# Optimization experiments

Measured on AMD Instinct MI355X. Metric: run time of the kernel, lower is better.

The kernel has to match this reference:

```python
import jax, jax.numpy as jnp
import numpy as np

HEADS, DK, S, SIGMA = 8, 64, 48, 5.0  # d_model=512, query/key spatial 48x48


def setup_inputs() -> dict:
    rng = jax.random.key(0)
    ks = jax.random.split(rng, 8)
    b, n, d = 2, S * S, HEADS * DK
    sc = 0.03  # keep pre-softmax scores in a sane range
    return {
        "query": jax.random.normal(ks[0], (b, n, d), jnp.float32),
        "key": jax.random.normal(ks[1], (b, n, d), jnp.float32),
        "value0": jax.random.uniform(ks[2], (b, n), jnp.float32),
        "value1": jax.random.uniform(ks[3], (b, n), jnp.float32),
        "Wq": jax.random.normal(ks[4], (d, d), jnp.float32) * sc,
        "bq": jax.random.normal(ks[5], (d,), jnp.float32) * sc,
        "Wk": jax.random.normal(ks[6], (d, d), jnp.float32) * sc,
        "bk": jax.random.normal(ks[7], (d,), jnp.float32) * sc,
    }


def _apply_gaussian_kernel(corr):
    # corr: [B, hw, S, S]  (B = b*heads, hw = S*S query positions)
    B = corr.shape[0]
    idx = jnp.argmax(corr, axis=1)                       # [B, S, S] best query index per key pos
    idx_y = (idx // S).astype(corr.dtype)[:, None, None, :, :]  # [B,1,1,S,S]
    idx_x = (idx % S).astype(corr.dtype)[:, None, None, :, :]
    lin = jnp.linspace(-1.0, 1.0, S).astype(corr.dtype)
    x = lin.reshape(1, 1, S, 1, 1)
    y = lin.reshape(1, S, 1, 1, 1)
    # faithful to source: linspace grid vs integer argmax coords
    gk = jnp.exp(-((x - idx_x) ** 2 + (y - idx_y) ** 2) / (2.0 * SIGMA ** 2))  # [B,S,S,S,S]
    return gk.reshape(B, S * S, S, S) * corr


def reference(query, key, value0, value1, Wq, bq, Wk, bk):
    b, nq, d = query.shape
    q = (query @ Wq.T + bq).reshape(b, nq, HEADS, DK).transpose(0, 2, 1, 3)  # [b,h,nq,dk]
    k = (key @ Wk.T + bk).reshape(b, -1, HEADS, DK).transpose(0, 2, 1, 3)    # [b,h,nk,dk]
    scores = jnp.einsum('bhqd,bhkd->bhqk', q, k)                             # [b,h,nq,nk]
    B = b * HEADS
    corr = _apply_gaussian_kernel(scores.reshape(B, nq, S, S))
    scores = corr.reshape(b, HEADS, nq, nq) / jnp.sqrt(jnp.asarray(DK, scores.dtype))
    attn = jax.nn.softmax(scores, axis=-1)
    x0 = jnp.einsum('bhqk,bk->bhq', attn, value0)   # attn @ value0
    x1 = jnp.einsum('bhqk,bq->bhk', attn, value1)   # attn^T @ value1
    # outer product per head, then mean over heads -> [b,nq,nk]
    return jnp.einsum('bhq,bhk->bqk', x0, x1) / HEADS
```

## Files before the change

kernel.cpp:

```cpp
#include <hip/hip_runtime.h>
#include <cstddef>
#include <cstdint>

namespace {

constexpr int S = 48;
constexpr int N = S * S;
constexpr int D = 512;
constexpr int DK = 64;
constexpr int B = 2;
constexpr int BH = 16;
constexpr int BHN = BH * N;
constexpr int G_ARG = 9;
constexpr int CH_ARG = N / G_ARG;
constexpr int G_RC = 6;
constexpr int CH_RC = N / G_RC;
constexpr float SCALE = 0.125f;
constexpr float INV2S2 = 0.02f;

typedef __attribute__((ext_vector_type(8))) short short8;
typedef __attribute__((ext_vector_type(8))) unsigned short ushort8v;
typedef __attribute__((ext_vector_type(4))) float f32x4;

#define MFMA(a, b, c) __builtin_amdgcn_mfma_f32_16x16x32_bf16((a), (b), (c), 0, 0, 0)

struct U3 { ushort a, b, c; };

__device__ __forceinline__ U3 split3(float x)
{
    U3 u;
    uint b1 = __float_as_uint(x);
    uint r1 = (b1 + (0x7FFFu + ((b1 >> 16) & 1u))) & 0xFFFF0000u;
    u.a = (ushort)(r1 >> 16);
    float d1 = x - __uint_as_float(r1);
    uint b2 = __float_as_uint(d1);
    uint r2 = (b2 + (0x7FFFu + ((b2 >> 16) & 1u))) & 0xFFFF0000u;
    u.b = (ushort)(r2 >> 16);
    float d2 = d1 - __uint_as_float(r2);
    uint b3 = __float_as_uint(d2);
    u.c = (ushort)((b3 + (0x7FFFu + ((b3 >> 16) & 1u))) >> 16);
    return u;
}

__device__ __forceinline__ void stage_async(ushort* __restrict__ L,
                                            const ushort* __restrict__ g, int tid)
{
    #pragma unroll
    for (int it = 0; it < 2; it++) {
        int f = tid + 256 * it;
        int row = f >> 3, c8 = (f & 7) * 8;
        int srcoff = row * 64 + (c8 ^ ((row & 7) << 3));
        ushort* lbase = L + (size_t)(f & ~63) * 8;
        __builtin_amdgcn_global_load_lds(
            (const __attribute__((address_space(1))) void*)(g + srcoff),
            (__attribute__((address_space(3))) void*)lbase, 16, 0, 0);
    }
}

__device__ __forceinline__ short8 frag_swz(const ushort* __restrict__ L, int row, int k)
{
    int off = row * 64 + (k ^ ((row & 7) << 3));
    return *(const short8*)&L[off];
}

__device__ __forceinline__ short8 gfrag(const ushort* __restrict__ p, size_t off)
{
    return *(const short8*)&p[off];
}

__global__ __launch_bounds__(256)
void split_kernel(const float* __restrict__ qin, const float* __restrict__ kin,
                  const float* __restrict__ Wq, const float* __restrict__ Wk,
                  ushort* __restrict__ XQ1, ushort* __restrict__ XQ2, ushort* __restrict__ XQ3,
                  ushort* __restrict__ XK1, ushort* __restrict__ XK2, ushort* __restrict__ XK3,
                  ushort* __restrict__ W1, ushort* __restrict__ W2, ushort* __restrict__ W3)
{
    const int z = blockIdx.y;
    const int gid = blockIdx.x * 256 + threadIdx.x;
    const float* src;
    ushort *O1, *O2, *O3;
    size_t dst, soff;
    if (z < 2) {
        int m = gid >> 6, c = gid & 63;
        int b = (m >= N) ? 1 : 0;
        int npos = m - b * N;
        src = z ? kin : qin;
        if (z) { O1 = XK1; O2 = XK2; O3 = XK3; }
        else   { O1 = XQ1; O2 = XQ2; O3 = XQ3; }
        soff = (size_t)m * D + c * 8;
        dst = ((size_t)(b * 8 + (c >> 3)) * N + npos) * 64 + (c & 7) * 8;
    } else {
        if (gid >= 65536) return;
        int r = gid >> 6, c = gid & 63;
        int inp = r >> 9, n = r & 511;
        src = inp ? Wk : Wq;
        O1 = W1; O2 = W2; O3 = W3;
        soff = (size_t)n * D + c * 8;
        dst = ((size_t)(inp * 8 + (c >> 3)) * 512 + n) * 64 + (c & 7) * 8;
    }
    ushort8v u1, u2, u3;
    #pragma unroll
    for (int j = 0; j < 8; j++) {
        U3 t = split3(src[soff + j]);
        u1[j] = t.a; u2[j] = t.b; u3[j] = t.c;
    }
    *(ushort8v*)&O1[dst] = u1;
    *(ushort8v*)&O2[dst] = u2;
    *(ushort8v*)&O3[dst] = u3;
}

__global__ __launch_bounds__(256)
void proj_kernel(const ushort* __restrict__ X1, const ushort* __restrict__ X2,
                 const ushort* __restrict__ X3, const ushort* __restrict__ Wp1,
                 const ushort* __restrict__ Wp2, const ushort* __restrict__ Wp3,
                 const float* __restrict__ bias,
                 ushort* __restrict__ O1, ushort* __restrict__ O2, ushort* __restrict__ O3)
{
    const int tid = threadIdx.x;
    const int lane = tid & 63, w = tid >> 6;
    const int wm = w >> 1, wn = w & 1;
    const int lg = lane >> 4, ln = lane & 15;
    const int hsel = blockIdx.x;
    const int my = blockIdx.y;
    const int b = my / 36;
    const int npos0 = (my % 36) * 64;

    __shared__ alignas(16) ushort bufX[3][64 * 64];
    __shared__ alignas(16) ushort bufW[3][64 * 64];

    f32x4 acc[2][2];
    #pragma unroll
    for (int mt = 0; mt < 2; mt++)
        #pragma unroll
        for (int nt = 0; nt < 2; nt++) acc[mt][nt] = (f32x4){0.f, 0.f, 0.f, 0.f};

    for (int kh = 0; kh < 8; kh++) {
        stage_async(bufX[0], X1 + ((size_t)(b * 8 + kh) * N + npos0) * 64, tid);
        stage_async(bufX[1], X2 + ((size_t)(b * 8 + kh) * N + npos0) * 64, tid);
        stage_async(bufX[2], X3 + ((size_t)(b * 8 + kh) * N + npos0) * 64, tid);
        stage_async(bufW[0], Wp1 + ((size_t)kh * 512 + hsel * 64) * 64, tid);
        stage_async(bufW[1], Wp2 + ((size_t)kh * 512 + hsel * 64) * 64, tid);
        stage_async(bufW[2], Wp3 + ((size_t)kh * 512 + hsel * 64) * 64, tid);
        __syncthreads();

        short8 A[3][2][2], Bv[3][2][2];
        #pragma unroll
        for (int mt = 0; mt < 2; mt++)
            #pragma unroll
            for (int c = 0; c < 2; c++) {
                int row = 32 * wm + 16 * mt + ln, k = 32 * c + 8 * lg;
                A[0][mt][c] = frag_swz(bufX[0], row, k);
                A[1][mt][c] = frag_swz(bufX[1], row, k);
                A[2][mt][c] = frag_swz(bufX[2], row, k);
            }
        #pragma unroll
        for (int nt = 0; nt < 2; nt++)
            #pragma unroll
            for (int c = 0; c < 2; c++) {
                int row = 32 * wn + 16 * nt + ln, k = 32 * c + 8 * lg;
                Bv[0][nt][c] = frag_swz(bufW[0], row, k);
                Bv[1][nt][c] = frag_swz(bufW[1], row, k);
                Bv[2][nt][c] = frag_swz(bufW[2], row, k);
            }
        #pragma unroll
        for (int mt = 0; mt < 2; mt++)
            #pragma unroll
            for (int nt = 0; nt < 2; nt++) {
                f32x4 a = acc[mt][nt];
                a = MFMA(A[0][mt][0], Bv[0][nt][0], a);
                a = MFMA(A[0][mt][1], Bv[0][nt][1], a);
                a = MFMA(A[0][mt][0], Bv[1][nt][0], a);
                a = MFMA(A[0][mt][1], Bv[1][nt][1], a);
                a = MFMA(A[1][mt][0], Bv[0][nt][0], a);
                a = MFMA(A[1][mt][1], Bv[0][nt][1], a);
                a = MFMA(A[0][mt][0], Bv[2][nt][0], a);
                a = MFMA(A[0][mt][1], Bv[2][nt][1], a);
                a = MFMA(A[1][mt][0], Bv[1][nt][0], a);
                a = MFMA(A[1][mt][1], Bv[1][nt][1], a);
                a = MFMA(A[2][mt][0], Bv[0][nt][0], a);
                a = MFMA(A[2][mt][1], Bv[0][nt][1], a);
                acc[mt][nt] = a;
            }
        __syncthreads();
    }
    float* Cs = (float*)&bufX[0][0];
    #pragma unroll
    for (int mt = 0; mt < 2; mt++)
        #pragma unroll
        for (int nt = 0; nt < 2; nt++)
            #pragma unroll
            for (int r = 0; r < 4; r++)
                Cs[(32 * wm + 16 * mt + 4 * lg + r) * 68 + 32 * wn + 16 * nt + ln] =
                    acc[mt][nt][r];
    __syncthreads();
    const int row = tid >> 2, c0 = (tid & 3) * 16;
    size_t dst = ((size_t)(b * 8 + hsel) * N + npos0 + row) * 64 + c0;
    #pragma unroll
    for (int half = 0; half < 2; half++) {
        ushort8v u1, u2, u3;
        #pragma unroll
        for (int j = 0; j < 8; j++) {
            int cc = c0 + half * 8 + j;
            float v = Cs[row * 68 + cc] + bias[hsel * 64 + cc];
            U3 t = split3(v);
            u1[j] = t.a; u2[j] = t.b; u3[j] = t.c;
        }
        *(ushort8v*)&O1[dst + half * 8] = u1;
        *(ushort8v*)&O2[dst + half * 8] = u2;
        *(ushort8v*)&O3[dst + half * 8] = u3;
    }
}

__global__ __launch_bounds__(256)
void argmax_kernel(const ushort* __restrict__ Q1, const ushort* __restrict__ Q2,
                   const ushort* __restrict__ Q3, const ushort* __restrict__ K1,
                   const ushort* __restrict__ K2, const ushort* __restrict__ K3,
                   float* __restrict__ argV, int* __restrict__ argQ)
{
    const int bh = blockIdx.y;
    const int g  = blockIdx.z;
    const int tid = threadIdx.x;
    const int w = tid >> 6, lane = tid & 63;
    const int lg = lane >> 4, ln = lane & 15;
    const int kb = blockIdx.x * 128 + w * 32;
    const size_t hb = (size_t)bh * N;

    __shared__ alignas(16) ushort buf[3][64 * 64];

    short8 A[3][2][2];
    #pragma unroll
    for (int mt = 0; mt < 2; mt++)
        #pragma unroll
        for (int c = 0; c < 2; c++) {
            size_t off = (hb + kb + 16 * mt + ln) * 64 + 32 * c + 8 * lg;
            A[0][mt][c] = gfrag(K1, off);
            A[1][mt][c] = gfrag(K2, off);
            A[2][mt][c] = gfrag(K3, off);
        }

    float bestv[2][4];
    int   bestq[2][4];
    #pragma unroll
    for (int mt = 0; mt < 2; mt++)
        #pragma unroll
        for (int r = 0; r < 4; r++) { bestv[mt][r] = -3e38f; bestq[mt][r] = 0; }

    for (int qt = g * CH_ARG; qt < (g + 1) * CH_ARG; qt += 64) {
        stage_async(buf[0], Q1 + (hb + qt) * 64, tid);
        stage_async(buf[1], Q2 + (hb + qt) * 64, tid);
        stage_async(buf[2], Q3 + (hb + qt) * 64, tid);
        __syncthreads();
        #pragma unroll
        for (int nt = 0; nt < 4; nt++) {
            short8 Bv0[2], Bv1[2], Bv2[2];
            #pragma unroll
            for (int c = 0; c < 2; c++) {
                int row = 16 * nt + ln, k = 32 * c + 8 * lg;
                Bv0[c] = frag_swz(buf[0], row, k);
                Bv1[c] = frag_swz(buf[1], row, k);
                Bv2[c] = frag_swz(buf[2], row, k);
            }
            const int q = qt + 16 * nt + ln;
            #pragma unroll
            for (int mt = 0; mt < 2; mt++) {
                f32x4 acc = {0.f, 0.f, 0.f, 0.f};
                acc = MFMA(A[0][mt][0], Bv0[0], acc);
                acc = MFMA(A[0][mt][1], Bv0[1], acc);
                acc = MFMA(A[0][mt][0], Bv1[0], acc);
                acc = MFMA(A[0][mt][1], Bv1[1], acc);
                acc = MFMA(A[1][mt][0], Bv0[0], acc);
                acc = MFMA(A[1][mt][1], Bv0[1], acc);
                acc = MFMA(A[0][mt][0], Bv2[0], acc);
                acc = MFMA(A[0][mt][1], Bv2[1], acc);
                acc = MFMA(A[1][mt][0], Bv1[0], acc);
                acc = MFMA(A[1][mt][1], Bv1[1], acc);
                acc = MFMA(A[2][mt][0], Bv0[0], acc);
                acc = MFMA(A[2][mt][1], Bv0[1], acc);
                #pragma unroll
                for (int r = 0; r < 4; r++)
                    if (acc[r] > bestv[mt][r]) { bestv[mt][r] = acc[r]; bestq[mt][r] = q; }
            }
        }
        __syncthreads();
    }
    #pragma unroll
    for (int d = 1; d < 16; d <<= 1) {
        #pragma unroll
        for (int mt = 0; mt < 2; mt++)
            #pragma unroll
            for (int r = 0; r < 4; r++) {
                float ov = __shfl_xor(bestv[mt][r], d);
                int   oq = __shfl_xor(bestq[mt][r], d);
                if (ov > bestv[mt][r] || (ov == bestv[mt][r] && oq < bestq[mt][r])) {
                    bestv[mt][r] = ov; bestq[mt][r] = oq;
                }
            }
    }
    if (ln == 0) {
        #pragma unroll
        for (int mt = 0; mt < 2; mt++)
            #pragma unroll
            for (int r = 0; r < 4; r++) {
                size_t o = (size_t)g * BHN + hb + kb + 16 * mt + 4 * lg + r;
                argV[o] = bestv[mt][r];
                argQ[o] = bestq[mt][r];
            }
    }
}

__global__ __launch_bounds__(256)
void argcombine_kernel(const float* __restrict__ argV, const int* __restrict__ argQ,
                       int* __restrict__ idxout)
{
    int i = blockIdx.x * 256 + threadIdx.x;
    if (i >= BHN) return;
    float bv = argV[i]; int bq = argQ[i];
    #pragma unroll
    for (int g = 1; g < G_ARG; g++) {
        float v = argV[(size_t)g * BHN + i];
        int   q = argQ[(size_t)g * BHN + i];
        if (v > bv) { bv = v; bq = q; }
    }
    idxout[i] = bq;
}

__global__ __launch_bounds__(256)
void rowpass_kernel(const ushort* __restrict__ Q1, const ushort* __restrict__ Q2,
                    const ushort* __restrict__ K1, const ushort* __restrict__ K2,
                    const int* __restrict__ idxbuf, const float* __restrict__ value0,
                    float* __restrict__ rowPl, float* __restrict__ rowPa)
{
    const int bh = blockIdx.y, b = bh >> 3;
    const int g = blockIdx.z;
    const int tid = threadIdx.x;
    const int w = tid >> 6, lane = tid & 63;
    const int lg = lane >> 4, ln = lane & 15;
    const int qb = blockIdx.x * 128 + w * 32;
    const size_t hb = (size_t)bh * N;

    __shared__ alignas(16) ushort buf[2][64 * 64];
    __shared__ float F[48][49];
    __shared__ int ixi[64], iyi[64];
    __shared__ float v0s[64];

    for (int i = tid; i < 48 * 48; i += 256) {
        int a = i / 48, j = i % 48;
        float lj = -1.0f + (2.0f / 47.0f) * (float)j;
        float dd = lj - (float)a;
        F[a][j] = __expf(-dd * dd * INV2S2);
    }

    short8 Bq[2][2][2];
    int qx_[2], qy_[2];
    #pragma unroll
    for (int nt = 0; nt < 2; nt++) {
        #pragma unroll
        for (int c = 0; c < 2; c++) {
            size_t off = (hb + qb + 16 * nt + ln) * 64 + 32 * c + 8 * lg;
            Bq[0][nt][c] = gfrag(Q1, off);
            Bq[1][nt][c] = gfrag(Q2, off);
        }
        int qq = qb + 16 * nt + ln;
        qx_[nt] = qq % 48; qy_[nt] = qq / 48;
    }
    __syncthreads();

    float l[2] = {0.f, 0.f}, a0[2] = {0.f, 0.f};

    for (int kt = g * CH_RC; kt < (g + 1) * CH_RC; kt += 64) {
        stage_async(buf[0], K1 + (hb + kt) * 64, tid);
        stage_async(buf[1], K2 + (hb + kt) * 64, tid);
        if (tid < 64) {
            int v = idxbuf[hb + kt + tid];
            ixi[tid] = v % 48; iyi[tid] = v / 48;
            v0s[tid] = value0[(size_t)b * N + kt + tid];
        }
        __syncthreads();
        #pragma unroll
        for (int mt = 0; mt < 4; mt++) {
            short8 A0[2], A1[2];
            #pragma unroll
            for (int c = 0; c < 2; c++) {
                int row = 16 * mt + ln, k = 32 * c + 8 * lg;
                A0[c] = frag_swz(buf[0], row, k);
                A1[c] = frag_swz(buf[1], row, k);
            }
            #pragma unroll
            for (int nt = 0; nt < 2; nt++) {
                f32x4 acc = {0.f, 0.f, 0.f, 0.f};
                acc = MFMA(A0[0], Bq[0][nt][0], acc);
                acc = MFMA(A0[1], Bq[0][nt][1], acc);
                acc = MFMA(A0[0], Bq[1][nt][0], acc);
                acc = MFMA(A0[1], Bq[1][nt][1], acc);
                acc = MFMA(A1[0], Bq[0][nt][0], acc);
                acc = MFMA(A1[1], Bq[0][nt][1], acc);
                #pragma unroll
                for (int r = 0; r < 4; r++) {
                    int kl = 16 * mt + 4 * lg + r;
                    float s = acc[r] * F[ixi[kl]][qx_[nt]] * F[iyi[kl]][qy_[nt]] * SCALE;
                    float e = __expf(s);
                    l[nt]  += e;
                    a0[nt] += e * v0s[kl];
                }
            }
        }
        __syncthreads();
    }
    #pragma unroll
    for (int d = 16; d < 64; d <<= 1) {
        #pragma unroll
        for (int nt = 0; nt < 2; nt++) {
            l[nt]  += __shfl_xor(l[nt], d);
            a0[nt] += __shfl_xor(a0[nt], d);
        }
    }
    if (lane < 16) {
        #pragma unroll
        for (int nt = 0; nt < 2; nt++) {
            size_t o = (size_t)g * BHN + hb + qb + 16 * nt + ln;
            rowPl[o] = l[nt];
            rowPa[o] = a0[nt];
        }
    }
}

__global__ __launch_bounds__(256)
void rowfinal_kernel(const float* __restrict__ rowPl, const float* __restrict__ rowPa,
                     float* __restrict__ denomo, float* __restrict__ x0o)
{
    int i = blockIdx.x * 256 + threadIdx.x;
    if (i >= BHN) return;
    float L = 0.f, A = 0.f;
    #pragma unroll
    for (int g = 0; g < G_RC; g++) {
        L += rowPl[(size_t)g * BHN + i];
        A += rowPa[(size_t)g * BHN + i];
    }
    denomo[i] = L;
    x0o[i] = A / L;
}

__global__ __launch_bounds__(256)
void colpass_kernel(const ushort* __restrict__ Q1, const ushort* __restrict__ Q2,
                    const ushort* __restrict__ K1, const ushort* __restrict__ K2,
                    const int* __restrict__ idxbuf, const float* __restrict__ value1,
                    const float* __restrict__ denomo, float* __restrict__ colP)
{
    const int bh = blockIdx.y, b = bh >> 3;
    const int g = blockIdx.z;
    const int tid = threadIdx.x;
    const int w = tid >> 6, lane = tid & 63;
    const int lg = lane >> 4, ln = lane & 15;
    const int kb = blockIdx.x * 128 + w * 32;
    const size_t hb = (size_t)bh * N;

    __shared__ alignas(16) ushort buf[2][64 * 64];
    __shared__ float F[48][49];
    __shared__ float wvs[64];
    __shared__ int qxs[64], qys[64];

    for (int i = tid; i < 48 * 48; i += 256) {
        int a = i / 48, j = i % 48;
        float lj = -1.0f + (2.0f / 47.0f) * (float)j;
        float dd = lj - (float)a;
        F[a][j] = __expf(-dd * dd * INV2S2);
    }

    short8 A[2][2][2];
    int ixr[2][4], iyr[2][4];
    #pragma unroll
    for (int mt = 0; mt < 2; mt++) {
        #pragma unroll
        for (int c = 0; c < 2; c++) {
            size_t off = (hb + kb + 16 * mt + ln) * 64 + 32 * c + 8 * lg;
            A[0][mt][c] = gfrag(K1, off);
            A[1][mt][c] = gfrag(K2, off);
        }
        int4 iv = *(const int4*)&idxbuf[hb + kb + 16 * mt + 4 * lg];
        ixr[mt][0] = iv.x % 48; iyr[mt][0] = iv.x / 48;
        ixr[mt][1] = iv.y % 48; iyr[mt][1] = iv.y / 48;
        ixr[mt][2] = iv.z % 48; iyr[mt][2] = iv.z / 48;
        ixr[mt][3] = iv.w % 48; iyr[mt][3] = iv.w / 48;
    }
    __syncthreads();

    float acc1[2][4] = {};

    for (int qt = g * CH_RC; qt < (g + 1) * CH_RC; qt += 64) {
        stage_async(buf[0], Q1 + (hb + qt) * 64, tid);
        stage_async(buf[1], Q2 + (hb + qt) * 64, tid);
        if (tid < 64) {
            int qg = qt + tid;
            wvs[tid] = value1[(size_t)b * N + qg] / denomo[hb + qg];
            qxs[tid] = qg % 48; qys[tid] = qg / 48;
        }
        __syncthreads();
        #pragma unroll
        for (int nt = 0; nt < 4; nt++) {
            short8 B0[2], B1[2];
            #pragma unroll
            for (int c = 0; c < 2; c++) {
                int row = 16 * nt + ln, k = 32 * c + 8 * lg;
                B0[c] = frag_swz(buf[0], row, k);
                B1[c] = frag_swz(buf[1], row, k);
            }
            const int qi = 16 * nt + ln;
            const int qx = qxs[qi], qy = qys[qi];
            const float wv = wvs[qi];
            #pragma unroll
            for (int mt = 0; mt < 2; mt++) {
                f32x4 acc = {0.f, 0.f, 0.f, 0.f};
                acc = MFMA(A[0][mt][0], B0[0], acc);
                acc = MFMA(A[0][mt][1], B0[1], acc);
                acc = MFMA(A[0][mt][0], B1[0], acc);
                acc = MFMA(A[0][mt][1], B1[1], acc);
                acc = MFMA(A[1][mt][0], B0[0], acc);
                acc = MFMA(A[1][mt][1], B0[1], acc);
                #pragma unroll
                for (int r = 0; r < 4; r++) {
                    float s = acc[r] * F[ixr[mt][r]][qx] * F[iyr[mt][r]][qy] * SCALE;
                    acc1[mt][r] += __expf(s) * wv;
                }
            }
        }
        __syncthreads();
    }
    #pragma unroll
    for (int d = 1; d < 16; d <<= 1)
        #pragma unroll
        for (int mt = 0; mt < 2; mt++)
            #pragma unroll
            for (int r = 0; r < 4; r++)
                acc1[mt][r] += __shfl_xor(acc1[mt][r], d);
    if (ln == 0) {
        #pragma unroll
        for (int mt = 0; mt < 2; mt++)
            #pragma unroll
            for (int r = 0; r < 4; r++)
                colP[(size_t)g * BHN + hb + kb + 16 * mt + 4 * lg + r] = acc1[mt][r];
    }
}

__global__ __launch_bounds__(256)
void colfinal_kernel(const float* __restrict__ colP, float* __restrict__ x1o)
{
    int i = blockIdx.x * 256 + threadIdx.x;
    if (i >= BHN) return;
    float X = 0.f;
    #pragma unroll
    for (int g = 0; g < G_RC; g++) X += colP[(size_t)g * BHN + i];
    x1o[i] = X;
}

__global__ __launch_bounds__(256)
void outer_kernel(const float* __restrict__ x0, const float* __restrict__ x1,
                  float* __restrict__ out)
{
    const int b = blockIdx.z;
    const int q0 = blockIdx.y * 32, k0 = blockIdx.x * 32;
    __shared__ float x0s[8][32];
    __shared__ float x1s[8][32];
    const int tid = threadIdx.x;
    {
        int hh = tid >> 5, i = tid & 31;
        x0s[hh][i] = x0[(size_t)(b * 8 + hh) * N + q0 + i];
        x1s[hh][i] = x1[(size_t)(b * 8 + hh) * N + k0 + i];
    }
    __syncthreads();
    const int row = tid >> 3, c4 = (tid & 7) * 4;
    float4 a = {0.f, 0.f, 0.f, 0.f};
    #pragma unroll
    for (int hh = 0; hh < 8; hh++) {
        float s = x0s[hh][row];
        a.x += s * x1s[hh][c4 + 0];
        a.y += s * x1s[hh][c4 + 1];
        a.z += s * x1s[hh][c4 + 2];
        a.w += s * x1s[hh][c4 + 3];
    }
    a.x *= 0.125f; a.y *= 0.125f; a.z *= 0.125f; a.w *= 0.125f;
    *(float4*)(out + (size_t)b * N * N + (size_t)(q0 + row) * N + k0 + c4) = a;
}

}

extern "C" void kernel_launch(void* const* d_in, const int* in_sizes, int n_in,
                              void* d_out, int out_size, void* d_ws, size_t ws_size,
                              hipStream_t stream) {
    const float* qin = (const float*)d_in[0];
    const float* kin = (const float*)d_in[1];
    const float* v0  = (const float*)d_in[2];
    const float* v1  = (const float*)d_in[3];
    const float* Wq  = (const float*)d_in[4];
    const float* bq  = (const float*)d_in[5];
    const float* Wk  = (const float*)d_in[6];
    const float* bk  = (const float*)d_in[7];
    float* out = (float*)d_out;

    const size_t ARR = (size_t)BH * N * DK;
    ushort* out_u = (ushort*)d_out;
    ushort* Q1  = out_u;
    ushort* Q2  = out_u + ARR;
    ushort* Q3  = out_u + 2 * ARR;
    ushort* XK1 = out_u + 3 * ARR;
    ushort* XK2 = out_u + 4 * ARR;
    ushort* XK3 = out_u + 5 * ARR;
    ushort* XQ1 = out_u + 6 * ARR;
    ushort* XQ2 = out_u + 7 * ARR;
    ushort* XQ3 = out_u + 8 * ARR;
    ushort* K1 = XQ1;  ushort* K2 = XQ2;  ushort* K3 = XQ3;

    float* tail = (float*)XK1;
    float* argV  = tail;
    int*   argQ  = (int*)(argV + (size_t)G_ARG * BHN);
    float* rowPl = (float*)(argQ + (size_t)G_ARG * BHN);
    float* rowPa = rowPl + (size_t)G_RC * BHN;
    float* colP  = rowPa + (size_t)G_RC * BHN;
    int*   idxb  = (int*)(colP + (size_t)G_RC * BHN);
    float* den   = (float*)(idxb + (size_t)BHN);

    const size_t WARR = (size_t)2 * 512 * 512;
    ushort* W1 = (ushort*)d_ws;
    ushort* W2 = W1 + WARR;
    ushort* W3 = W2 + WARR;
    float* x0b = (float*)(W3 + WARR);
    float* x1b = x0b + (size_t)BHN;

    const size_t WSLICE = (size_t)8 * 512 * 64;

    const int RB = (BHN + 255) / 256;

    split_kernel     <<<dim3(1152, 3),       dim3(256), 0, stream>>>(qin, kin, Wq, Wk,
                                                                     XQ1, XQ2, XQ3,
                                                                     XK1, XK2, XK3,
                                                                     W1, W2, W3);
    proj_kernel      <<<dim3(8, 72),         dim3(256), 0, stream>>>(XQ1, XQ2, XQ3,
                                                                     W1, W2, W3, bq,
                                                                     Q1, Q2, Q3);
    proj_kernel      <<<dim3(8, 72),         dim3(256), 0, stream>>>(XK1, XK2, XK3,
                                                                     W1 + WSLICE, W2 + WSLICE,
                                                                     W3 + WSLICE, bk,
                                                                     K1, K2, K3);
    argmax_kernel    <<<dim3(18, 16, G_ARG), dim3(256), 0, stream>>>(Q1, Q2, Q3, K1, K2, K3,
                                                                     argV, argQ);
    argcombine_kernel<<<dim3(RB),            dim3(256), 0, stream>>>(argV, argQ, idxb);
    rowpass_kernel   <<<dim3(18, 16, G_RC),  dim3(256), 0, stream>>>(Q1, Q2, K1, K2, idxb, v0,
                                                                     rowPl, rowPa);
    rowfinal_kernel  <<<dim3(RB),            dim3(256), 0, stream>>>(rowPl, rowPa, den, x0b);
    colpass_kernel   <<<dim3(18, 16, G_RC),  dim3(256), 0, stream>>>(Q1, Q2, K1, K2, idxb, v1,
                                                                     den, colP);
    colfinal_kernel  <<<dim3(RB),            dim3(256), 0, stream>>>(colP, x1b);
    outer_kernel     <<<dim3(72, 72, 2),     dim3(256), 0, stream>>>(x0b, x1b, out);
}
```

Baseline: 243.1 us.

## Double-buffer LDS staging and fold softmax scale into exp2 Gaussian table

Argmax, rowpass and colpass kernels now prefetch the next Q/K tile into a second LDS buffer while computing on the current one, with one barrier per iteration. The per-chunk index, coordinate and value tables are preloaded once for the whole chunk instead of per tile. The score scale and log2(e) are folded into the Gaussian table so the inner loop uses a raw exp2. This raises LDS usage per block and may lower occupancy.

```diff
diff --git a/kernel.cpp b/kernel.cpp
--- a/kernel.cpp
+++ b/kernel.cpp
@@ -17,6 +17,7 @@
 constexpr int CH_RC = N / G_RC;
 constexpr float SCALE = 0.125f;
 constexpr float INV2S2 = 0.02f;
+constexpr float FC = 0.42466080f;
 
 typedef __attribute__((ext_vector_type(8))) short short8;
 typedef __attribute__((ext_vector_type(8))) unsigned short ushort8v;
@@ -66,6 +67,13 @@
 __device__ __forceinline__ short8 gfrag(const ushort* __restrict__ p, size_t off)
 {
     return *(const short8*)&p[off];
+}
+
+__device__ __forceinline__ void pipe_barrier()
+{
+    asm volatile("s_waitcnt vmcnt(0) lgkmcnt(0)" ::: "memory");
+    __builtin_amdgcn_s_barrier();
+    __builtin_amdgcn_sched_barrier(0);
 }
 
 __global__ __launch_bounds__(256)
@@ -224,8 +232,9 @@
     const int lg = lane >> 4, ln = lane & 15;
     const int kb = blockIdx.x * 128 + w * 32;
     const size_t hb = (size_t)bh * N;
-
-    __shared__ alignas(16) ushort buf[3][64 * 64];
+    const int qbase = g * CH_ARG;
+
+    __shared__ alignas(16) ushort buf[2][3][64 * 64];
 
     short8 A[3][2][2];
     #pragma unroll
@@ -245,22 +254,30 @@
         #pragma unroll
         for (int r = 0; r < 4; r++) { bestv[mt][r] = -3e38f; bestq[mt][r] = 0; }
 
-    for (int qt = g * CH_ARG; qt < (g + 1) * CH_ARG; qt += 64) {
-        stage_async(buf[0], Q1 + (hb + qt) * 64, tid);
-        stage_async(buf[1], Q2 + (hb + qt) * 64, tid);
-        stage_async(buf[2], Q3 + (hb + qt) * 64, tid);
-        __syncthreads();
+    stage_async(buf[0][0], Q1 + (hb + qbase) * 64, tid);
+    stage_async(buf[0][1], Q2 + (hb + qbase) * 64, tid);
+    stage_async(buf[0][2], Q3 + (hb + qbase) * 64, tid);
+    pipe_barrier();
+
+    const int NT = CH_ARG / 64;
+    int cur = 0;
+    for (int t = 0; t < NT; ++t) {
+        if (t + 1 < NT) {
+            stage_async(buf[cur ^ 1][0], Q1 + (hb + qbase + (t + 1) * 64) * 64, tid);
+            stage_async(buf[cur ^ 1][1], Q2 + (hb + qbase + (t + 1) * 64) * 64, tid);
+            stage_async(buf[cur ^ 1][2], Q3 + (hb + qbase + (t + 1) * 64) * 64, tid);
+        }
         #pragma unroll
         for (int nt = 0; nt < 4; nt++) {
             short8 Bv0[2], Bv1[2], Bv2[2];
             #pragma unroll
             for (int c = 0; c < 2; c++) {
                 int row = 16 * nt + ln, k = 32 * c + 8 * lg;
-                Bv0[c] = frag_swz(buf[0], row, k);
-                Bv1[c] = frag_swz(buf[1], row, k);
-                Bv2[c] = frag_swz(buf[2], row, k);
-            }
-            const int q = qt + 16 * nt + ln;
+                Bv0[c] = frag_swz(buf[cur][0], row, k);
+                Bv1[c] = frag_swz(buf[cur][1], row, k);
+                Bv2[c] = frag_swz(buf[cur][2], row, k);
+            }
+            const int q = qbase + t * 64 + 16 * nt + ln;
             #pragma unroll
             for (int mt = 0; mt < 2; mt++) {
                 f32x4 acc = {0.f, 0.f, 0.f, 0.f};
@@ -281,7 +298,8 @@
                     if (acc[r] > bestv[mt][r]) { bestv[mt][r] = acc[r]; bestq[mt][r] = q; }
             }
         }
-        __syncthreads();
+        pipe_barrier();
+        cur ^= 1;
     }
     #pragma unroll
     for (int d = 1; d < 16; d <<= 1) {
@@ -337,17 +355,23 @@
     const int lg = lane >> 4, ln = lane & 15;
     const int qb = blockIdx.x * 128 + w * 32;
     const size_t hb = (size_t)bh * N;
-
-    __shared__ alignas(16) ushort buf[2][64 * 64];
+    const int kbase = g * CH_RC;
+
+    __shared__ alignas(16) ushort buf[2][2][64 * 64];
     __shared__ float F[48][49];
-    __shared__ int ixi[64], iyi[64];
-    __shared__ float v0s[64];
+    __shared__ int ixi[CH_RC], iyi[CH_RC];
+    __shared__ float v0s[CH_RC];
 
     for (int i = tid; i < 48 * 48; i += 256) {
         int a = i / 48, j = i % 48;
         float lj = -1.0f + (2.0f / 47.0f) * (float)j;
         float dd = lj - (float)a;
-        F[a][j] = __expf(-dd * dd * INV2S2);
+        F[a][j] = __expf(-dd * dd * INV2S2) * FC;
+    }
+    for (int i = tid; i < CH_RC; i += 256) {
+        int v = idxbuf[hb + kbase + i];
+        ixi[i] = v % 48; iyi[i] = v / 48;
+        v0s[i] = value0[(size_t)b * N + kbase + i];
     }
 
     short8 Bq[2][2][2];
@@ -363,27 +387,27 @@
         int qq = qb + 16 * nt + ln;
         qx_[nt] = qq % 48; qy_[nt] = qq / 48;
     }
-    __syncthreads();
+
+    stage_async(buf[0][0], K1 + (hb + kbase) * 64, tid);
+    stage_async(buf[0][1], K2 + (hb + kbase) * 64, tid);
+    pipe_barrier();
 
     float l[2] = {0.f, 0.f}, a0[2] = {0.f, 0.f};
-
-    for (int kt = g * CH_RC; kt < (g + 1) * CH_RC; kt += 64) {
-        stage_async(buf[0], K1 + (hb + kt) * 64, tid);
-        stage_async(buf[1], K2 + (hb + kt) * 64, tid);
-        if (tid < 64) {
-            int v = idxbuf[hb + kt + tid];
-            ixi[tid] = v % 48; iyi[tid] = v / 48;
-            v0s[tid] = value0[(size_t)b * N + kt + tid];
-        }
-        __syncthreads();
+    const int NT = CH_RC / 64;
+    int cur = 0;
+    for (int t = 0; t < NT; ++t) {
+        if (t + 1 < NT) {
+            stage_async(buf[cur ^ 1][0], K1 + (hb + kbase + (t + 1) * 64) * 64, tid);
+            stage_async(buf[cur ^ 1][1], K2 + (hb + kbase + (t + 1) * 64) * 64, tid);
+        }
         #pragma unroll
         for (int mt = 0; mt < 4; mt++) {
             short8 A0[2], A1[2];
             #pragma unroll
             for (int c = 0; c < 2; c++) {
                 int row = 16 * mt + ln, k = 32 * c + 8 * lg;
-                A0[c] = frag_swz(buf[0], row, k);
-                A1[c] = frag_swz(buf[1], row, k);
+                A0[c] = frag_swz(buf[cur][0], row, k);
+                A1[c] = frag_swz(buf[cur][1], row, k);
             }
             #pragma unroll
             for (int nt = 0; nt < 2; nt++) {
@@ -396,15 +420,16 @@
                 acc = MFMA(A1[1], Bq[0][nt][1], acc);
                 #pragma unroll
                 for (int r = 0; r < 4; r++) {
-                    int kl = 16 * mt + 4 * lg + r;
-                    float s = acc[r] * F[ixi[kl]][qx_[nt]] * F[iyi[kl]][qy_[nt]] * SCALE;
-                    float e = __expf(s);
+                    int koff = t * 64 + 16 * mt + 4 * lg + r;
+                    float tt = acc[r] * F[ixi[koff]][qx_[nt]] * F[iyi[koff]][qy_[nt]];
+                    float e = __builtin_amdgcn_exp2f(tt);
                     l[nt]  += e;
-                    a0[nt] += e * v0s[kl];
+                    a0[nt] += e * v0s[koff];
                 }
             }
         }
-        __syncthreads();
+        pipe_barrier();
+        cur ^= 1;
     }
     #pragma unroll
     for (int d = 16; d < 64; d <<= 1) {
@@ -453,17 +478,23 @@
     const int lg = lane >> 4, ln = lane & 15;
     const int kb = blockIdx.x * 128 + w * 32;
     const size_t hb = (size_t)bh * N;
-
-    __shared__ alignas(16) ushort buf[2][64 * 64];
+    const int qbase = g * CH_RC;
+
+    __shared__ alignas(16) ushort buf[2][2][64 * 64];
     __shared__ float F[48][49];
-    __shared__ float wvs[64];
-    __shared__ int qxs[64], qys[64];
+    __shared__ float wvs[CH_RC];
+    __shared__ int qxs[CH_RC], qys[CH_RC];
 
     for (int i = tid; i < 48 * 48; i += 256) {
         int a = i / 48, j = i % 48;
         float lj = -1.0f + (2.0f / 47.0f) * (float)j;
         float dd = lj - (float)a;
-        F[a][j] = __expf(-dd * dd * INV2S2);
+        F[a][j] = __expf(-dd * dd * INV2S2) * FC;
+    }
+    for (int i = tid; i < CH_RC; i += 256) {
+        int qg = qbase + i;
+        wvs[i] = value1[(size_t)b * N + qg] / denomo[hb + qg];
+        qxs[i] = qg % 48; qys[i] = qg / 48;
     }
 
     short8 A[2][2][2];
@@ -482,31 +513,31 @@
         ixr[mt][2] = iv.z % 48; iyr[mt][2] = iv.z / 48;
         ixr[mt][3] = iv.w % 48; iyr[mt][3] = iv.w / 48;
     }
-    __syncthreads();
+
+    stage_async(buf[0][0], Q1 + (hb + qbase) * 64, tid);
+    stage_async(buf[0][1], Q2 + (hb + qbase) * 64, tid);
+    pipe_barrier();
 
     float acc1[2][4] = {};
-
-    for (int qt = g * CH_RC; qt < (g + 1) * CH_RC; qt += 64) {
-        stage_async(buf[0], Q1 + (hb + qt) * 64, tid);
-        stage_async(buf[1], Q2 + (hb + qt) * 64, tid);
-        if (tid < 64) {
-            int qg = qt + tid;
-            wvs[tid] = value1[(size_t)b * N + qg] / denomo[hb + qg];
-            qxs[tid] = qg % 48; qys[tid] = qg / 48;
-        }
-        __syncthreads();
+    const int NT = CH_RC / 64;
+    int cur = 0;
+    for (int t = 0; t < NT; ++t) {
+        if (t + 1 < NT) {
+            stage_async(buf[cur ^ 1][0], Q1 + (hb + qbase + (t + 1) * 64) * 64, tid);
+            stage_async(buf[cur ^ 1][1], Q2 + (hb + qbase + (t + 1) * 64) * 64, tid);
+        }
         #pragma unroll
         for (int nt = 0; nt < 4; nt++) {
             short8 B0[2], B1[2];
             #pragma unroll
             for (int c = 0; c < 2; c++) {
                 int row = 16 * nt + ln, k = 32 * c + 8 * lg;
-                B0[c] = frag_swz(buf[0], row, k);
-                B1[c] = frag_swz(buf[1], row, k);
-            }
-            const int qi = 16 * nt + ln;
-            const int qx = qxs[qi], qy = qys[qi];
-            const float wv = wvs[qi];
+                B0[c] = frag_swz(buf[cur][0], row, k);
+                B1[c] = frag_swz(buf[cur][1], row, k);
+            }
+            const int qoff = t * 64 + 16 * nt + ln;
+            const int qx = qxs[qoff], qy = qys[qoff];
+            const float wv = wvs[qoff];
             #pragma unroll
             for (int mt = 0; mt < 2; mt++) {
                 f32x4 acc = {0.f, 0.f, 0.f, 0.f};
@@ -518,12 +549,13 @@
                 acc = MFMA(A[1][mt][1], B0[1], acc);
                 #pragma unroll
                 for (int r = 0; r < 4; r++) {
-                    float s = acc[r] * F[ixr[mt][r]][qx] * F[iyr[mt][r]][qy] * SCALE;
-                    acc1[mt][r] += __expf(s) * wv;
+                    float tt = acc[r] * F[ixr[mt][r]][qx] * F[iyr[mt][r]][qy];
+                    acc1[mt][r] += __builtin_amdgcn_exp2f(tt) * wv;
                 }
             }
         }
-        __syncthreads();
+        pipe_barrier();
+        cur ^= 1;
     }
     #pragma unroll
     for (int d = 1; d < 16; d <<= 1)
```

Result: slower. 260.0 us (+6.9%).
